# Kernel optimization log

Measured on AMD Instinct MI355X. Metric: run time of the kernel, lower is better.

The kernel has to match this reference:

```python
import jax, jax.numpy as jnp
import numpy as np

B, T, C = 4, 2048, 1024
H = 16
D = C // H  # head_dim = 64


def setup_inputs() -> dict:
    key = jax.random.key(0)
    ks = jax.random.split(key, 3)
    scale = 1.0 / np.sqrt(C)
    x = jax.random.normal(ks[0], (B, T, C), dtype=jnp.float32)
    w_qkv = jax.random.normal(ks[1], (C, 3 * C), dtype=jnp.float32) * scale
    b_qkv = jnp.zeros((3 * C,), dtype=jnp.float32)
    w_proj = jax.random.normal(ks[2], (C, C), dtype=jnp.float32) * scale
    b_proj = jnp.zeros((C,), dtype=jnp.float32)
    return {"x": x, "w_qkv": w_qkv, "b_qkv": b_qkv, "w_proj": w_proj, "b_proj": b_proj}


def reference(x, w_qkv, b_qkv, w_proj, b_proj):
    # qkv projection: [B,T,3C]
    qkv = x @ w_qkv + b_qkv
    q, k, v = jnp.split(qkv, 3, axis=-1)
    # [B,T,C] -> [B,H,T,D]
    q = q.reshape(B, T, H, D).transpose(0, 2, 1, 3)
    k = k.reshape(B, T, H, D).transpose(0, 2, 1, 3)
    v = v.reshape(B, T, H, D).transpose(0, 2, 1, 3)
    # scores [B,H,T,T] with causal mask
    att = jnp.einsum('bhqd,bhkd->bhqk', q, k) / jnp.sqrt(jnp.float32(D))
    causal = jnp.tril(jnp.ones((T, T), dtype=bool))
    att = jnp.where(causal[None, None], att, -jnp.inf)
    att = jax.nn.softmax(att, axis=-1)
    y = jnp.einsum('bhqk,bhkd->bhqd', att, v)
    y = y.transpose(0, 2, 1, 3).reshape(B, T, C)
    return y @ w_proj + b_proj
```

## Files before the change

kernel.cpp:

```cpp
#include <hip/hip_runtime.h>

#define B_ 4
#define T_ 2048
#define C_ 1024
#define H_ 16
#define D_ 64

typedef unsigned short u16;
typedef unsigned int u32;
typedef __bf16 bf16x8 __attribute__((ext_vector_type(8)));
typedef float f32x4 __attribute__((ext_vector_type(4)));

__device__ __forceinline__ u16 f2bf(float f) {
  union { float fv; unsigned u; } v; v.fv = f;
  unsigned r = v.u + 0x7FFFu + ((v.u >> 16) & 1u);
  return (u16)(r >> 16);
}
__device__ __forceinline__ u32 fbits(float f) {
  union { float fv; u32 u; } v; v.fv = f; return v.u;
}
__device__ __forceinline__ u32 pkbf(float lo, float hi) {
  return __builtin_amdgcn_perm(fbits(hi), fbits(lo), 0x07060302u);
}

__device__ __forceinline__ void gld_lds16(const u16* g, u16* l) {
  __builtin_amdgcn_global_load_lds((const __attribute__((address_space(1))) unsigned*)(const void*)g,
                                   (__attribute__((address_space(3))) unsigned*)(void*)l, 16, 0, 0);
}

__global__ __launch_bounds__(256) void cvt_bf16_k(const float* __restrict__ in,
                                                  u16* __restrict__ out, int n4) {
  int i = blockIdx.x * 256 + threadIdx.x;
  if (i < n4) {
    float4 v = ((const float4*)in)[i];
    ushort4 o;
    o.x = f2bf(v.x); o.y = f2bf(v.y); o.z = f2bf(v.z); o.w = f2bf(v.w);
    ((ushort4*)out)[i] = o;
  }
}

__global__ __launch_bounds__(256) void wtrans_k(const float* __restrict__ W,
                                                u16* __restrict__ Wt, int K, int N) {
  __shared__ float tile[32][33];
  int tx = threadIdx.x, ty = threadIdx.y;
  int n0 = blockIdx.x * 32, k0 = blockIdx.y * 32;
#pragma unroll
  for (int i = ty; i < 32; i += 8) tile[i][tx] = W[(size_t)(k0 + i) * N + n0 + tx];
  __syncthreads();
#pragma unroll
  for (int i = ty; i < 32; i += 8) Wt[(size_t)(n0 + i) * K + k0 + tx] = f2bf(tile[tx][i]);
}

template <int EPI>
__global__ __launch_bounds__(256) void gemm_bt_k(
    const u16* __restrict__ A, const u16* __restrict__ Bt, const float* __restrict__ bias,
    u16* __restrict__ Qb, u16* __restrict__ Kb, u16* __restrict__ Vt,
    float* __restrict__ Cout, int M, int N, int K) {
  __shared__ __attribute__((aligned(16))) u16 As[128 * 64];
  __shared__ __attribute__((aligned(16))) u16 Bs[128 * 64];
  int tid = threadIdx.x, wave = tid >> 6, lane = tid & 63;
  int c15 = lane & 15, quad = lane >> 4;
  int tM = blockIdx.y * 128, tN = blockIdx.x * 128;
  int moff = (wave & 1) * 64, noff = (wave >> 1) * 64;
  f32x4 acc[4][4] = {};

  for (int k0 = 0; k0 < K; k0 += 64) {
    __syncthreads();
#pragma unroll
    for (int i = 0; i < 4; i++) {
      int idx = i * 256 + tid;
      int row = idx >> 3, g = (idx & 7) ^ (row & 7);
      const u16* asrc;
      if (EPI == 2) {
        int m = tM + row, b = m >> 11, t = m & 2047;
        asrc = A + (((size_t)(b * H_ + (k0 >> 6)) * T_ + t) * D_ + g * 8);
      } else {
        asrc = A + (size_t)(tM + row) * K + k0 + g * 8;
      }
      gld_lds16(asrc, As + idx * 8);
      gld_lds16(Bt + (size_t)(tN + row) * K + k0 + g * 8, Bs + idx * 8);
    }
    __syncthreads();
#pragma unroll
    for (int ks = 0; ks < 64; ks += 32) {
      int ch = (ks >> 3) + quad;
      int sw = (ch ^ (c15 & 7)) << 3;
      bf16x8 af[4], bfr[4];
#pragma unroll
      for (int mf = 0; mf < 4; mf++)
        af[mf] = *(const bf16x8*)(As + (moff + mf * 16 + c15) * 64 + sw);
#pragma unroll
      for (int nf = 0; nf < 4; nf++)
        bfr[nf] = *(const bf16x8*)(Bs + (noff + nf * 16 + c15) * 64 + sw);
#pragma unroll
      for (int mf = 0; mf < 4; mf++)
#pragma unroll
        for (int nf = 0; nf < 4; nf++)
          acc[mf][nf] = __builtin_amdgcn_mfma_f32_16x16x32_bf16(af[mf], bfr[nf], acc[mf][nf], 0, 0, 0);
    }
  }

  const float SCLQ = 0.18033688011f;
#pragma unroll
  for (int nf = 0; nf < 4; nf++) {
    int n = tN + noff + nf * 16 + c15;
    float bsv = bias[n];
#pragma unroll
    for (int mf = 0; mf < 4; mf++) {
      int m0 = tM + moff + mf * 16 + quad * 4;
      if (EPI == 1) {
        int part = n >> 10, h = (n >> 6) & 15, d = n & 63;
        int b = m0 >> 11, t0 = m0 & 2047;
        if (part < 2) {
          u16* dst = (part == 0) ? Qb : Kb;
          float scl = (part == 0) ? SCLQ : 1.0f;
#pragma unroll
          for (int r = 0; r < 4; r++)
            dst[((size_t)(b * H_ + h) * T_ + t0 + r) * D_ + d] = f2bf((acc[mf][nf][r] + bsv) * scl);
        } else {
          ushort4 o;
          o.x = f2bf(acc[mf][nf][0] + bsv);
          o.y = f2bf(acc[mf][nf][1] + bsv);
          o.z = f2bf(acc[mf][nf][2] + bsv);
          o.w = f2bf(acc[mf][nf][3] + bsv);
          *(ushort4*)(Vt + ((size_t)(b * H_ + h) * D_ + d) * T_ + t0) = o;
        }
      } else {
#pragma unroll
        for (int r = 0; r < 4; r++)
          Cout[(size_t)(m0 + r) * N + n] = acc[mf][nf][r] + bsv;
      }
    }
  }
}

__global__ __launch_bounds__(256, 3) void attn_k(const u16* __restrict__ Qb,
                                                 const u16* __restrict__ Kb,
                                                 const u16* __restrict__ Vt,
                                                 u16* __restrict__ Yb) {
  constexpr int PD = 72;
  __shared__ __attribute__((aligned(16))) u16 Ps[128 * PD];
  int tid = threadIdx.x, wave = tid >> 6, lane = tid & 63;
  int c15 = lane & 15, quad = lane >> 4;
  int pairp = blockIdx.x, bh = blockIdx.y;
  const u16* Qg = Qb + (size_t)bh * T_ * D_;
  const u16* Kg = Kb + (size_t)bh * T_ * D_;
  const u16* Vg = Vt + (size_t)bh * D_ * T_;

  for (int half = 0; half < 2; half++) {
    int qt = half ? (15 - pairp) : pairp;
    int q0 = qt * 128;
    int nkt = 2 * qt + 2;
    __syncthreads();
#pragma unroll
    for (int i = 0; i < 4; i++) {
      int c = tid + i * 256, row = c >> 3, kc = c & 7;
      *(uint4*)(Ps + row * PD + kc * 8) = *(const uint4*)(Qg + (size_t)(q0 + row) * D_ + kc * 8);
    }
    __syncthreads();

    bf16x8 qf[2][2];
#pragma unroll
    for (int mq = 0; mq < 2; mq++)
#pragma unroll
      for (int ks = 0; ks < 2; ks++)
        qf[mq][ks] = *(const bf16x8*)(Ps + (wave * 32 + mq * 16 + c15) * PD + ks * 32 + quad * 8);

    float l_s[2] = {0.f, 0.f};
    f32x4 O[4][2] = {};

    for (int kt = 0; kt < nkt; kt++) {
      int k0 = kt * 64;
      bf16x8 kf[2][4], vf[2][4];
#pragma unroll
      for (int ks = 0; ks < 2; ks++)
#pragma unroll
        for (int nf = 0; nf < 4; nf++)
          kf[ks][nf] = *(const bf16x8*)(Kg + (size_t)(k0 + nf * 16 + c15) * D_ + ks * 32 + quad * 8);
#pragma unroll
      for (int ks = 0; ks < 2; ks++)
#pragma unroll
        for (int dt = 0; dt < 4; dt++)
          vf[ks][dt] = *(const bf16x8*)(Vg + (size_t)(dt * 16 + c15) * T_ + k0 + ks * 32 + quad * 8);

      f32x4 S[2][4] = {};
#pragma unroll
      for (int ks = 0; ks < 2; ks++)
#pragma unroll
        for (int mq = 0; mq < 2; mq++)
#pragma unroll
          for (int nf = 0; nf < 4; nf++)
            S[mq][nf] = __builtin_amdgcn_mfma_f32_16x16x32_bf16(kf[ks][nf], qf[mq][ks], S[mq][nf], 0, 0, 0);

      bool maskt = (k0 + 63 > q0);
#pragma unroll
      for (int mq = 0; mq < 2; mq++) {
        float sum = 0.f;
        if (maskt) {
          int q = q0 + wave * 32 + mq * 16 + c15;
#pragma unroll
          for (int nf = 0; nf < 4; nf++)
#pragma unroll
            for (int r = 0; r < 4; r++) {
              int key = k0 + nf * 16 + quad * 4 + r;
              float p = (key <= q) ? __builtin_amdgcn_exp2f(S[mq][nf][r]) : 0.f;
              S[mq][nf][r] = p;
              sum += p;
            }
        } else {
#pragma unroll
          for (int nf = 0; nf < 4; nf++)
#pragma unroll
            for (int r = 0; r < 4; r++) {
              float p = __builtin_amdgcn_exp2f(S[mq][nf][r]);
              S[mq][nf][r] = p;
              sum += p;
            }
        }
        l_s[mq] += sum;
      }

#pragma unroll
      for (int mq = 0; mq < 2; mq++) {
        int qrow = wave * 32 + mq * 16 + c15;
#pragma unroll
        for (int nf = 0; nf < 4; nf++) {
          uint2 o;
          o.x = pkbf(S[mq][nf][0], S[mq][nf][1]);
          o.y = pkbf(S[mq][nf][2], S[mq][nf][3]);
          *(uint2*)(Ps + qrow * PD + nf * 16 + quad * 4) = o;
        }
      }
      __asm__ volatile("" ::: "memory");

#pragma unroll
      for (int ks = 0; ks < 2; ks++) {
        bf16x8 pf[2];
#pragma unroll
        for (int mq = 0; mq < 2; mq++)
          pf[mq] = *(const bf16x8*)(Ps + (wave * 32 + mq * 16 + c15) * PD + ks * 32 + quad * 8);
#pragma unroll
        for (int dt = 0; dt < 4; dt++)
#pragma unroll
          for (int mq = 0; mq < 2; mq++)
            O[dt][mq] = __builtin_amdgcn_mfma_f32_16x16x32_bf16(vf[ks][dt], pf[mq], O[dt][mq], 0, 0, 0);
      }
    }

#pragma unroll
    for (int mq = 0; mq < 2; mq++) {
      float l = l_s[mq];
      l += __shfl_xor(l, 16, 64);
      l += __shfl_xor(l, 32, 64);
      float inv = 1.0f / l;
      int q = q0 + wave * 32 + mq * 16 + c15;
#pragma unroll
      for (int dt = 0; dt < 4; dt++) {
        ushort4 o;
        o.x = f2bf(O[dt][mq][0] * inv); o.y = f2bf(O[dt][mq][1] * inv);
        o.z = f2bf(O[dt][mq][2] * inv); o.w = f2bf(O[dt][mq][3] * inv);
        *(ushort4*)(Yb + ((size_t)bh * T_ + q) * D_ + dt * 16 + quad * 4) = o;
      }
    }
  }
}

extern "C" void kernel_launch(void* const* d_in, const int* in_sizes, int n_in,
                              void* d_out, int out_size, void* d_ws, size_t ws_size,
                              hipStream_t stream) {
  const float* x      = (const float*)d_in[0];
  const float* w_qkv  = (const float*)d_in[1];
  const float* b_qkv  = (const float*)d_in[2];
  const float* w_proj = (const float*)d_in[3];
  const float* b_proj = (const float*)d_in[4];
  float* out = (float*)d_out;
  char* ws = (char*)d_ws;
  const size_t MB = 1ull << 20;
  u16* W1t = (u16*)(ws + 0);
  u16* W2t = (u16*)(ws + 6 * MB);
  u16* Qb  = (u16*)(ws + 8 * MB);
  u16* Kb  = (u16*)(ws + 24 * MB);
  u16* Vt  = (u16*)(ws + 40 * MB);
  u16* Xb  = (u16*)((char*)d_out + 16 * MB);

  cvt_bf16_k<<<8192, 256, 0, stream>>>(x, Xb, (B_ * T_ * C_) / 4);
  wtrans_k<<<dim3(96, 32), dim3(32, 8), 0, stream>>>(w_qkv, W1t, C_, 3 * C_);
  wtrans_k<<<dim3(32, 32), dim3(32, 8), 0, stream>>>(w_proj, W2t, C_, C_);
  gemm_bt_k<1><<<dim3(24, 64), 256, 0, stream>>>(Xb, W1t, b_qkv, Qb, Kb, Vt, nullptr,
                                                 B_ * T_, 3 * C_, C_);
  attn_k<<<dim3(8, 64), 256, 0, stream>>>(Qb, Kb, Vt, Qb);
  gemm_bt_k<2><<<dim3(8, 64), 256, 0, stream>>>(Qb, W2t, b_proj, nullptr, nullptr, nullptr,
                                                out, B_ * T_, C_, C_);
}
```

Baseline: 313.8 us.

## Stage K and V tiles through double-buffered swizzled LDS with async loads

```diff
diff --git a/kernel.cpp b/kernel.cpp
--- a/kernel.cpp
+++ b/kernel.cpp
@@ -134,11 +134,13 @@
   }
 }
 
-__global__ __launch_bounds__(256, 3) void attn_k(const u16* __restrict__ Qb,
-                                                 const u16* __restrict__ Kb,
-                                                 const u16* __restrict__ Vt,
-                                                 u16* __restrict__ Yb) {
+__global__ __launch_bounds__(256) void attn_k(const u16* __restrict__ Qb,
+                                              const u16* __restrict__ Kb,
+                                              const u16* __restrict__ Vt,
+                                              u16* __restrict__ Yb) {
   constexpr int PD = 72;
+  __shared__ __attribute__((aligned(16))) u16 Ks[2 * 64 * 64];
+  __shared__ __attribute__((aligned(16))) u16 Vs[2 * 64 * 64];
   __shared__ __attribute__((aligned(16))) u16 Ps[128 * PD];
   int tid = threadIdx.x, wave = tid >> 6, lane = tid & 63;
   int c15 = lane & 15, quad = lane >> 4;
@@ -157,6 +159,12 @@
       int c = tid + i * 256, row = c >> 3, kc = c & 7;
       *(uint4*)(Ps + row * PD + kc * 8) = *(const uint4*)(Qg + (size_t)(q0 + row) * D_ + kc * 8);
     }
+#pragma unroll
+    for (int i = 0; i < 2; i++) {
+      int idx = i * 256 + tid, row = idx >> 3, g = (idx & 7) ^ (row & 7);
+      gld_lds16(Kg + (size_t)row * D_ + g * 8, Ks + idx * 8);
+      gld_lds16(Vg + (size_t)row * T_ + g * 8, Vs + idx * 8);
+    }
     __syncthreads();
 
     bf16x8 qf[2][2];
@@ -170,27 +178,37 @@
     f32x4 O[4][2] = {};
 
     for (int kt = 0; kt < nkt; kt++) {
+      int cur = kt & 1;
+      const u16* Ksb = Ks + cur * 4096;
+      const u16* Vsb = Vs + cur * 4096;
+      if (kt) __syncthreads();
+      if (kt + 1 < nkt) {
+        int k1 = (kt + 1) * 64;
+        u16* Kn = Ks + (cur ^ 1) * 4096;
+        u16* Vn = Vs + (cur ^ 1) * 4096;
+#pragma unroll
+        for (int i = 0; i < 2; i++) {
+          int idx = i * 256 + tid, row = idx >> 3, g = (idx & 7) ^ (row & 7);
+          gld_lds16(Kg + (size_t)(k1 + row) * D_ + g * 8, Kn + idx * 8);
+          gld_lds16(Vg + (size_t)row * T_ + k1 + g * 8, Vn + idx * 8);
+        }
+      }
       int k0 = kt * 64;
-      bf16x8 kf[2][4], vf[2][4];
-#pragma unroll
-      for (int ks = 0; ks < 2; ks++)
+
+      f32x4 S[2][4] = {};
+#pragma unroll
+      for (int ks = 0; ks < 2; ks++) {
+        int sw = (((ks << 2) + quad) ^ (c15 & 7)) << 3;
+        bf16x8 kf[4];
 #pragma unroll
         for (int nf = 0; nf < 4; nf++)
-          kf[ks][nf] = *(const bf16x8*)(Kg + (size_t)(k0 + nf * 16 + c15) * D_ + ks * 32 + quad * 8);
-#pragma unroll
-      for (int ks = 0; ks < 2; ks++)
-#pragma unroll
-        for (int dt = 0; dt < 4; dt++)
-          vf[ks][dt] = *(const bf16x8*)(Vg + (size_t)(dt * 16 + c15) * T_ + k0 + ks * 32 + quad * 8);
-
-      f32x4 S[2][4] = {};
-#pragma unroll
-      for (int ks = 0; ks < 2; ks++)
+          kf[nf] = *(const bf16x8*)(Ksb + (nf * 16 + c15) * 64 + sw);
 #pragma unroll
         for (int mq = 0; mq < 2; mq++)
 #pragma unroll
           for (int nf = 0; nf < 4; nf++)
-            S[mq][nf] = __builtin_amdgcn_mfma_f32_16x16x32_bf16(kf[ks][nf], qf[mq][ks], S[mq][nf], 0, 0, 0);
+            S[mq][nf] = __builtin_amdgcn_mfma_f32_16x16x32_bf16(kf[nf], qf[mq][ks], S[mq][nf], 0, 0, 0);
+      }
 
       bool maskt = (k0 + 63 > q0);
 #pragma unroll
@@ -235,7 +253,11 @@
 
 #pragma unroll
       for (int ks = 0; ks < 2; ks++) {
-        bf16x8 pf[2];
+        int sw = (((ks << 2) + quad) ^ (c15 & 7)) << 3;
+        bf16x8 vf[4], pf[2];
+#pragma unroll
+        for (int dt = 0; dt < 4; dt++)
+          vf[dt] = *(const bf16x8*)(Vsb + (dt * 16 + c15) * 64 + sw);
 #pragma unroll
         for (int mq = 0; mq < 2; mq++)
           pf[mq] = *(const bf16x8*)(Ps + (wave * 32 + mq * 16 + c15) * PD + ks * 32 + quad * 8);
@@ -243,7 +265,7 @@
         for (int dt = 0; dt < 4; dt++)
 #pragma unroll
           for (int mq = 0; mq < 2; mq++)
-            O[dt][mq] = __builtin_amdgcn_mfma_f32_16x16x32_bf16(vf[ks][dt], pf[mq], O[dt][mq], 0, 0, 0);
+            O[dt][mq] = __builtin_amdgcn_mfma_f32_16x16x32_bf16(vf[dt], pf[mq], O[dt][mq], 0, 0, 0);
       }
     }
 
```

Result: faster. 258.8 us (-17.5%).

## Merge prep kernels into one launch and prefetch next K tile in attention

Applied to the files above, without the earlier changes.

```diff
diff --git a/kernel.cpp b/kernel.cpp
--- a/kernel.cpp
+++ b/kernel.cpp
@@ -28,27 +28,30 @@
                                    (__attribute__((address_space(3))) unsigned*)(void*)l, 16, 0, 0);
 }
 
-__global__ __launch_bounds__(256) void cvt_bf16_k(const float* __restrict__ in,
-                                                  u16* __restrict__ out, int n4) {
-  int i = blockIdx.x * 256 + threadIdx.x;
-  if (i < n4) {
-    float4 v = ((const float4*)in)[i];
+__global__ __launch_bounds__(256) void prep_k(const float* __restrict__ x, u16* __restrict__ Xb,
+                                              const float* __restrict__ wq, u16* __restrict__ W1t,
+                                              const float* __restrict__ wp, u16* __restrict__ W2t) {
+  __shared__ float tile[32][33];
+  int bb = blockIdx.x, tid = threadIdx.x;
+  if (bb < 8192) {
+    int i = bb * 256 + tid;
+    float4 v = ((const float4*)x)[i];
     ushort4 o;
     o.x = f2bf(v.x); o.y = f2bf(v.y); o.z = f2bf(v.z); o.w = f2bf(v.w);
-    ((ushort4*)out)[i] = o;
+    ((ushort4*)Xb)[i] = o;
+  } else {
+    const float* W; u16* Wt; int N; int bidx;
+    if (bb < 8192 + 3072) { W = wq; Wt = W1t; N = 3 * C_; bidx = bb - 8192; }
+    else                  { W = wp; Wt = W2t; N = C_;     bidx = bb - 11264; }
+    int nb = N / 32;
+    int n0 = (bidx % nb) * 32, k0 = (bidx / nb) * 32;
+    int tx = tid & 31, ty = tid >> 5;
+#pragma unroll
+    for (int i = ty; i < 32; i += 8) tile[i][tx] = W[(size_t)(k0 + i) * N + n0 + tx];
+    __syncthreads();
+#pragma unroll
+    for (int i = ty; i < 32; i += 8) Wt[(size_t)(n0 + i) * C_ + k0 + tx] = f2bf(tile[tx][i]);
   }
-}
-
-__global__ __launch_bounds__(256) void wtrans_k(const float* __restrict__ W,
-                                                u16* __restrict__ Wt, int K, int N) {
-  __shared__ float tile[32][33];
-  int tx = threadIdx.x, ty = threadIdx.y;
-  int n0 = blockIdx.x * 32, k0 = blockIdx.y * 32;
-#pragma unroll
-  for (int i = ty; i < 32; i += 8) tile[i][tx] = W[(size_t)(k0 + i) * N + n0 + tx];
-  __syncthreads();
-#pragma unroll
-  for (int i = ty; i < 32; i += 8) Wt[(size_t)(n0 + i) * K + k0 + tx] = f2bf(tile[tx][i]);
 }
 
 template <int EPI>
@@ -134,10 +137,10 @@
   }
 }
 
-__global__ __launch_bounds__(256, 3) void attn_k(const u16* __restrict__ Qb,
-                                                 const u16* __restrict__ Kb,
-                                                 const u16* __restrict__ Vt,
-                                                 u16* __restrict__ Yb) {
+__global__ __launch_bounds__(256) void attn_k(const u16* __restrict__ Qb,
+                                              const u16* __restrict__ Kb,
+                                              const u16* __restrict__ Vt,
+                                              u16* __restrict__ Yb) {
   constexpr int PD = 72;
   __shared__ __attribute__((aligned(16))) u16 Ps[128 * PD];
   int tid = threadIdx.x, wave = tid >> 6, lane = tid & 63;
@@ -152,6 +155,14 @@
     int q0 = qt * 128;
     int nkt = 2 * qt + 2;
     __syncthreads();
+
+    bf16x8 kfA[2][4], kfB[2][4];
+#pragma unroll
+    for (int ks = 0; ks < 2; ks++)
+#pragma unroll
+      for (int nf = 0; nf < 4; nf++)
+        kfA[ks][nf] = *(const bf16x8*)(Kg + (size_t)(nf * 16 + c15) * D_ + ks * 32 + quad * 8);
+
 #pragma unroll
     for (int i = 0; i < 4; i++) {
       int c = tid + i * 256, row = c >> 3, kc = c & 7;
@@ -169,19 +180,22 @@
     float l_s[2] = {0.f, 0.f};
     f32x4 O[4][2] = {};
 
-    for (int kt = 0; kt < nkt; kt++) {
+    auto iter = [&](int kt, bf16x8 (&kfc)[2][4], bf16x8 (&kfn)[2][4]) {
       int k0 = kt * 64;
-      bf16x8 kf[2][4], vf[2][4];
-#pragma unroll
-      for (int ks = 0; ks < 2; ks++)
-#pragma unroll
-        for (int nf = 0; nf < 4; nf++)
-          kf[ks][nf] = *(const bf16x8*)(Kg + (size_t)(k0 + nf * 16 + c15) * D_ + ks * 32 + quad * 8);
+      bf16x8 vf[2][4];
 #pragma unroll
       for (int ks = 0; ks < 2; ks++)
 #pragma unroll
         for (int dt = 0; dt < 4; dt++)
           vf[ks][dt] = *(const bf16x8*)(Vg + (size_t)(dt * 16 + c15) * T_ + k0 + ks * 32 + quad * 8);
+      if (kt + 1 < nkt) {
+        int k1 = k0 + 64;
+#pragma unroll
+        for (int ks = 0; ks < 2; ks++)
+#pragma unroll
+          for (int nf = 0; nf < 4; nf++)
+            kfn[ks][nf] = *(const bf16x8*)(Kg + (size_t)(k1 + nf * 16 + c15) * D_ + ks * 32 + quad * 8);
+      }
 
       f32x4 S[2][4] = {};
 #pragma unroll
@@ -190,7 +204,7 @@
         for (int mq = 0; mq < 2; mq++)
 #pragma unroll
           for (int nf = 0; nf < 4; nf++)
-            S[mq][nf] = __builtin_amdgcn_mfma_f32_16x16x32_bf16(kf[ks][nf], qf[mq][ks], S[mq][nf], 0, 0, 0);
+            S[mq][nf] = __builtin_amdgcn_mfma_f32_16x16x32_bf16(kfc[ks][nf], qf[mq][ks], S[mq][nf], 0, 0, 0);
 
       bool maskt = (k0 + 63 > q0);
 #pragma unroll
@@ -245,6 +259,11 @@
           for (int mq = 0; mq < 2; mq++)
             O[dt][mq] = __builtin_amdgcn_mfma_f32_16x16x32_bf16(vf[ks][dt], pf[mq], O[dt][mq], 0, 0, 0);
       }
+    };
+
+    for (int kt = 0; kt < nkt; kt += 2) {
+      iter(kt, kfA, kfB);
+      iter(kt + 1, kfB, kfA);
     }
 
 #pragma unroll
@@ -283,9 +302,7 @@
   u16* Vt  = (u16*)(ws + 40 * MB);
   u16* Xb  = (u16*)((char*)d_out + 16 * MB);
 
-  cvt_bf16_k<<<8192, 256, 0, stream>>>(x, Xb, (B_ * T_ * C_) / 4);
-  wtrans_k<<<dim3(96, 32), dim3(32, 8), 0, stream>>>(w_qkv, W1t, C_, 3 * C_);
-  wtrans_k<<<dim3(32, 32), dim3(32, 8), 0, stream>>>(w_proj, W2t, C_, C_);
+  prep_k<<<12288, 256, 0, stream>>>(x, Xb, w_qkv, W1t, w_proj, W2t);
   gemm_bt_k<1><<<dim3(24, 64), 256, 0, stream>>>(Xb, W1t, b_qkv, Qb, Kb, Vt, nullptr,
                                                  B_ * T_, 3 * C_, C_);
   attn_k<<<dim3(8, 64), 256, 0, stream>>>(Qb, Kb, Vt, Qb);
```

Measured after the change: 323.7 us. 3.2% more time.
